# Performance work log

Hardware: AMD Instinct MI355X
Metric: run time of the kernel (lower is better)

## Reference

```python
import jax, jax.numpy as jnp
import numpy as np

NUM_ROUTES = 3
EPS = 1e-8

def _squash(s):
    # s: [b, out_caps, out_dim]
    n = jnp.linalg.norm(s, axis=-1, keepdims=True)
    scale = n ** 2 / (1.0 + n ** 2)
    return scale * (s / (n + EPS))

def setup_inputs() -> dict:
    key = jax.random.key(0)
    kx, kw = jax.random.split(key)
    B, IN_CAPS, IN_DIM, OUT_CAPS, OUT_DIM = 32, 2048, 16, 64, 32
    x = jax.random.normal(kx, (B, IN_CAPS, IN_DIM), dtype=jnp.float32)
    W = jax.random.normal(kw, (1, IN_CAPS, OUT_CAPS, OUT_DIM, IN_DIM), dtype=jnp.float32)
    return {"x": x, "W": W}

def reference(x, W):
    # u_hat[b,i,o,d] = sum_k W[0,i,o,d,k] * x[b,i,k]
    u_hat = jnp.einsum('iodk,bik->biod', W[0], x)  # [B, in_caps, out_caps, out_dim]
    b_ij = jnp.zeros(u_hat.shape[:3], dtype=u_hat.dtype)  # [B, in_caps, out_caps]
    v_j = None
    for _ in range(NUM_ROUTES):
        c_ij = jax.nn.softmax(b_ij, axis=2)
        s_j = jnp.einsum('bio,biod->bod', c_ij, u_hat)  # weighted sum over in_caps
        v_j = _squash(s_j)
        agreement = jnp.einsum('biod,bod->bio', u_hat, v_j)
        b_ij = b_ij + agreement
    return v_j
```

## Files before the change

### kernel.cpp

```cpp
#include <hip/hip_runtime.h>
#include <cstdint>

#define NB 32
#define IC 2048
#define IK 16
#define OC 64
#define OD 32
#define ODF (OC*OD)
#define PARTBLK (16*ODF)
#define NCH 128
#define NSLOT (NCH*2)

typedef __fp16 h2 __attribute__((ext_vector_type(2)));
typedef __fp16 h8 __attribute__((ext_vector_type(8)));
typedef float  f4 __attribute__((ext_vector_type(4)));

__device__ __forceinline__ h2 pk2(float a, float b) {
#if __has_builtin(__builtin_amdgcn_cvt_pkrtz)
  return __builtin_amdgcn_cvt_pkrtz(a, b);
#else
  h2 r; r.x = (__fp16)a; r.y = (__fp16)b; return r;
#endif
}
__device__ __forceinline__ float fdot2a(h2 a, h2 b, float c) {
#if __has_builtin(__builtin_amdgcn_fdot2)
  return __builtin_amdgcn_fdot2(a, b, c, false);
#else
  return c + (float)a.x*(float)b.x + (float)a.y*(float)b.y;
#endif
}
__device__ __forceinline__ unsigned int bcu(h2 v){ return __builtin_bit_cast(unsigned int, v); }
__device__ __forceinline__ h2 bch2(unsigned int u){ return __builtin_bit_cast(h2, u); }
__device__ __forceinline__ h8 bch8(uint4 u){ return __builtin_bit_cast(h8, u); }
__device__ __forceinline__ f4 mfma_16x16x32(h8 a, h8 b, f4 c) {
  return __builtin_amdgcn_mfma_f32_16x16x32_f16(a, b, c, 0, 0, 0);
}
__device__ __forceinline__ uint4 packw(const float* wp) {
  const float4 wa = *(const float4*)wp;
  const float4 wb = *(const float4*)(wp + 4);
  uint4 au;
  au.x = bcu(pk2(wa.x, wa.y)); au.y = bcu(pk2(wa.z, wa.w));
  au.z = bcu(pk2(wb.x, wb.y)); au.w = bcu(pk2(wb.z, wb.w));
  return au;
}


template<int WH>
__global__ __launch_bounds__(1024)
void caps_gemm0(const float* __restrict__ xg, const float* __restrict__ Wg,
                uint4* __restrict__ Whg, float* __restrict__ part)
{
  __shared__ uint4 x_h[8][2][16];
  const int t = threadIdx.x, w = t >> 6, l = t & 63, lb = l & 15, lg = l >> 4;
  const int bid = blockIdx.x, slot = bid >> 3;
  const int bh = slot & 1;
  const int ci = (bid & 7)*16 + (slot >> 1);
  const int i0 = ci*16, bg0 = bh*16;
  const f4 zf = {0.f,0.f,0.f,0.f};
  f4 acc[8];
#pragma unroll
  for (int q = 0; q < 8; ++q) acc[q] = zf;

  for (int g8 = 0; g8 < 16; g8 += 8) {
    if (g8) __syncthreads();
    if (t < 256) {
      const int si = t >> 5, kc2 = (t >> 4) & 1, sb = t & 15;
      const float* xp = &xg[((size_t)(bg0 + sb)*IC + (i0 + g8 + si))*IK + kc2*8];
      x_h[si][kc2][sb] = packw(xp);
    }
    __syncthreads();
#pragma unroll 1
    for (int p = 0; p < 4; ++p) {
      const int isel = lg >> 1, kc = lg & 1, il = p*2 + isel;
      const h8 B = bch8(x_h[il][kc][lb]);
#pragma unroll
      for (int tt = 0; tt < 8; ++tt) {
        const size_t widx = (size_t)(i0 + g8 + il)*ODF + (w*8 + tt)*16 + lb;
        const uint4 au = packw(&Wg[widx*IK + kc*8]);
        if (WH && bh == 0) Whg[widx*2 + kc] = au;
        acc[tt] = mfma_16x16x32(bch8(au), B, acc[tt]);
      }
    }
  }
  float* pp = part + (size_t)(ci*2 + bh)*PARTBLK;
#pragma unroll
  for (int tt = 0; tt < 8; ++tt) {
    float4 st;
    st.x = acc[tt].x*(1.f/64.f); st.y = acc[tt].y*(1.f/64.f);
    st.z = acc[tt].z*(1.f/64.f); st.w = acc[tt].w*(1.f/64.f);
    *(float4*)&pp[(size_t)lb*ODF + (w*8 + tt)*16 + lg*4] = st;
  }
}

template<int ITER, int WH>
__global__ __launch_bounds__(1024)
void caps_agree(const float* __restrict__ xg, const float* __restrict__ Wg,
                const uint4* __restrict__ Whg, const float* __restrict__ vin,
                float* __restrict__ a1g, float* __restrict__ cg)
{
  __shared__ uint4 x_h[8][2][16];
  __shared__ float agr[8*64*17];
  const int t = threadIdx.x, w = t >> 6, l = t & 63, lb = l & 15, lg = l >> 4;
  const int bid = blockIdx.x, slot = bid >> 3;
  const int bh = slot & 1;
  const int ci8 = (bid & 7)*32 + (slot >> 1);
  const int i0 = ci8*8, bg0 = bh*16;
  const f4 zf = {0.f,0.f,0.f,0.f};

  if (t < 256) {
    const int si = t >> 5, kc2 = (t >> 4) & 1, sb = t & 15;
    const float* xp = &xg[((size_t)(bg0 + sb)*IC + (i0 + si))*IK + kc2*8];
    x_h[si][kc2][sb] = packw(xp);
  }
  unsigned int vh[16];
#pragma unroll
  for (int tt = 0; tt < 8; ++tt) {
    const int o = w*4 + (tt >> 1);
    const float4 vv = *(const float4*)
      &vin[((size_t)(bg0 + lb)*OC + o)*OD + (tt & 1)*16 + lg*4];
    vh[tt*2]   = bcu(pk2(0.5f*vv.x, 0.5f*vv.y));
    vh[tt*2+1] = bcu(pk2(0.5f*vv.z, 0.5f*vv.w));
  }
  __syncthreads();

  const int isel = lg >> 1, kc = lg & 1;
  const unsigned int msk = (lg >= 2) ? 0x80008000u : 0u;

#pragma unroll 1
  for (int p = 0; p < 4; ++p) {
    const int iA = i0 + p*2, iB = iA + 1;
    const uint4 bu = x_h[p*2 + isel][kc][lb];
    uint4 bm;
    bm.x = bu.x^msk; bm.y = bu.y^msk; bm.z = bu.z^msk; bm.w = bu.w^msk;
    const h8 Bp = bch8(bu), Bm = bch8(bm);
    float ap1[4] = {0.f,0.f,0.f,0.f}, ap2[4] = {0.f,0.f,0.f,0.f};
#pragma unroll
    for (int tt = 0; tt < 8; ++tt) {
      const size_t widx = (size_t)(iA + isel)*ODF + (w*8 + tt)*16 + lb;
      const uint4 au = WH ? Whg[widx*2 + kc] : packw(&Wg[widx*IK + kc*8]);
      const h8 A = bch8(au);
      const f4 s = mfma_16x16x32(A, Bp, zf);
      const f4 d = mfma_16x16x32(A, Bm, zf);
      const h2 sh0 = pk2(s.x, s.y), sh1 = pk2(s.z, s.w);
      const h2 dh0 = pk2(d.x, d.y), dh1 = pk2(d.z, d.w);
      const float ds = fdot2a(sh0, bch2(vh[tt*2]), fdot2a(sh1, bch2(vh[tt*2+1]), 0.f));
      const float dd = fdot2a(dh0, bch2(vh[tt*2]), fdot2a(dh1, bch2(vh[tt*2+1]), 0.f));
      ap1[tt >> 1] += ds + dd;
      ap2[tt >> 1] += ds - dd;
    }
#pragma unroll
    for (int q = 0; q < 4; ++q) {
      float a1v = ap1[q], a2v = ap2[q];
      a1v += __shfl_xor(a1v, 16); a1v += __shfl_xor(a1v, 32);
      a2v += __shfl_xor(a2v, 16); a2v += __shfl_xor(a2v, 32);
      if (l < 16) {
        const int o = w*4 + q;
        float b1 = a1v, b2 = a2v;
        if (ITER == 2) {
          b1 += a1g[((size_t)iA*OC + o)*NB + bg0 + lb];
          b2 += a1g[((size_t)iB*OC + o)*NB + bg0 + lb];
        }
        if (ITER == 1) {
          a1g[((size_t)iA*OC + o)*NB + bg0 + lb] = b1;
          a1g[((size_t)iB*OC + o)*NB + bg0 + lb] = b2;
        }
        agr[((p*2)*64 + o)*17 + lb]   = b1;
        agr[((p*2+1)*64 + o)*17 + lb] = b2;
      }
    }
  }
  __syncthreads();
#pragma unroll
  for (int r = 0; r < 8; ++r) {
    const int row = w*8 + r, si = row >> 4, b = row & 15;
    const float a = agr[(si*64 + l)*17 + b];
    float m = a;
#pragma unroll
    for (int off = 1; off < 64; off <<= 1) m = fmaxf(m, __shfl_xor(m, off));
    const float e = __expf(a - m);
    float se = e;
#pragma unroll
    for (int off = 1; off < 64; off <<= 1) se += __shfl_xor(se, off);
    agr[(si*64 + l)*17 + b] = e / se;
  }
  __syncthreads();
#pragma unroll
  for (int cc = 0; cc < 8; ++cc) {
    const int o = t >> 4, b2 = t & 15;
    cg[((size_t)(i0 + cc)*OC + o)*NB + bg0 + b2] = agr[(cc*64 + o)*17 + b2];
  }
}

template<int WH>
__global__ __launch_bounds__(1024)
void caps_saccum(const float* __restrict__ xg, const float* __restrict__ Wg,
                 const uint4* __restrict__ Whg, const float* __restrict__ cg,
                 float* __restrict__ part)
{
  __shared__ uint4 x_h[8][2][16];
  const int t = threadIdx.x, w = t >> 6, l = t & 63, lb = l & 15, lg = l >> 4;
  const int bid = blockIdx.x, slot = bid >> 3;
  const int bh = slot & 1;
  const int ci = (bid & 7)*16 + (slot >> 1);
  const int i0 = ci*16, bg0 = bh*16;
  const f4 zf = {0.f,0.f,0.f,0.f};
  f4 acc[8];
#pragma unroll
  for (int q = 0; q < 8; ++q) acc[q] = zf;
  const int isel = lg >> 1, kc = lg & 1;

  for (int g8 = 0; g8 < 16; g8 += 8) {
    if (g8) __syncthreads();
    if (t < 256) {
      const int si = t >> 5, kc2 = (t >> 4) & 1, sb = t & 15;
      const float* xp = &xg[((size_t)(bg0 + sb)*IC + (i0 + g8 + si))*IK + kc2*8];
      x_h[si][kc2][sb] = packw(xp);
    }
    __syncthreads();
#pragma unroll 1
    for (int p = 0; p < 4; ++p) {
      const int iA = i0 + g8 + p*2, iB = iA + 1;
      const uint4 bu = x_h[p*2 + isel][kc][lb];
#pragma unroll
      for (int q = 0; q < 4; ++q) {
        const int o = w*4 + q;
        const float c1 = cg[((size_t)iA*OC + o)*NB + bg0 + lb];
        const float c2 = cg[((size_t)iB*OC + o)*NB + bg0 + lb];
        const float cs = (lg < 2) ? c1 : c2;
        const h2 cpk = pk2(cs, cs);
        uint4 bs;
        bs.x = bcu(bch2(bu.x)*cpk); bs.y = bcu(bch2(bu.y)*cpk);
        bs.z = bcu(bch2(bu.z)*cpk); bs.w = bcu(bch2(bu.w)*cpk);
        const h8 Bs = bch8(bs);
#pragma unroll
        for (int th = 0; th < 2; ++th) {
          const int tt = q*2 + th;
          const size_t widx = (size_t)(iA + isel)*ODF + (w*8 + tt)*16 + lb;
          const uint4 au = WH ? Whg[widx*2 + kc] : packw(&Wg[widx*IK + kc*8]);
          acc[tt] = mfma_16x16x32(bch8(au), Bs, acc[tt]);
        }
      }
    }
  }
  float* pp = part + (size_t)(ci*2 + bh)*PARTBLK;
#pragma unroll
  for (int tt = 0; tt < 8; ++tt) {
    float4 st; st.x = acc[tt].x; st.y = acc[tt].y; st.z = acc[tt].z; st.w = acc[tt].w;
    *(float4*)&pp[(size_t)lb*ODF + (w*8 + tt)*16 + lg*4] = st;
  }
}

__global__ __launch_bounds__(64)
void caps_reduce(const float* __restrict__ part, float* __restrict__ vout)
{
  const int r  = blockIdx.x;
  const int b  = r >> 6, o = r & 63;
  const int bh = b >> 4, bl = b & 15;
  const int d  = threadIdx.x & 31;
  const int h  = threadIdx.x >> 5;
  const float* p = part + (size_t)bh*PARTBLK + (size_t)bl*ODF + o*OD + d;
  float s = 0.f;
#pragma unroll 4
  for (int q = 0; q < NCH/2; ++q)
    s += p[(size_t)((h*(NCH/2) + q)*2)*PARTBLK];
  s += __shfl_xor(s, 32);
  float n2 = s*s;
#pragma unroll
  for (int off = 1; off < 32; off <<= 1) n2 += __shfl_xor(n2, off);
  const float n = sqrtf(n2);
  const float f = n2 / ((1.f + n2)*(n + 1e-8f));
  if (h == 0) vout[(size_t)r*OD + d] = s*f;
}

extern "C" void kernel_launch(void* const* d_in, const int* in_sizes, int n_in,
                              void* d_out, int out_size, void* d_ws, size_t ws_size,
                              hipStream_t stream)
{
  const float* xg = (const float*)d_in[0];
  const float* Wg = (const float*)d_in[1];
  float* out = (float*)d_out;

  const size_t part_b = (size_t)NSLOT*PARTBLK*sizeof(float);
  const size_t a1_b   = (size_t)IC*OC*NB*sizeof(float);
  const size_t c_b    = a1_b;
  const size_t v_b    = (size_t)NB*ODF*sizeof(float);
  const size_t wh_b   = (size_t)IC*ODF*IK*2;

  char* ws = (char*)d_ws;
  float* part = (float*)ws;                  ws += part_b;
  float* a1g  = (float*)ws;                  ws += a1_b;
  float* cg   = (float*)ws;                  ws += c_b;
  float* vbuf = (float*)ws;                  ws += v_b;
  uint4* whg  = (uint4*)ws;
  const bool WH = (part_b + a1_b + c_b + v_b + wh_b) <= ws_size;

  if (WH) {
    caps_gemm0<1><<<NSLOT, 1024, 0, stream>>>(xg, Wg, whg, part);
    caps_reduce<<<NB*OC, 64, 0, stream>>>(part, vbuf);
    caps_agree<1,1><<<512, 1024, 0, stream>>>(xg, Wg, whg, vbuf, a1g, cg);
    caps_saccum<1><<<NSLOT, 1024, 0, stream>>>(xg, Wg, whg, cg, part);
    caps_reduce<<<NB*OC, 64, 0, stream>>>(part, vbuf);
    caps_agree<2,1><<<512, 1024, 0, stream>>>(xg, Wg, whg, vbuf, a1g, cg);
    caps_saccum<1><<<NSLOT, 1024, 0, stream>>>(xg, Wg, whg, cg, part);
    caps_reduce<<<NB*OC, 64, 0, stream>>>(part, out);
  } else {
    caps_gemm0<0><<<NSLOT, 1024, 0, stream>>>(xg, Wg, nullptr, part);
    caps_reduce<<<NB*OC, 64, 0, stream>>>(part, vbuf);
    caps_agree<1,0><<<512, 1024, 0, stream>>>(xg, Wg, nullptr, vbuf, a1g, cg);
    caps_saccum<0><<<NSLOT, 1024, 0, stream>>>(xg, Wg, nullptr, cg, part);
    caps_reduce<<<NB*OC, 64, 0, stream>>>(part, vbuf);
    caps_agree<2,0><<<512, 1024, 0, stream>>>(xg, Wg, nullptr, vbuf, a1g, cg);
    caps_saccum<0><<<NSLOT, 1024, 0, stream>>>(xg, Wg, nullptr, cg, part);
    caps_reduce<<<NB*OC, 64, 0, stream>>>(part, out);
  }
}
```

Baseline: 286.7 us.

## Retile caps_saccum so each block covers all 32 batches over a quarter of outputs

caps_saccum changes from blocks covering 16 batches by all 64 output capsules to blocks covering all 32 batches by a quarter of the output tiles, with 512 blocks instead of 256. Each W fragment loaded from memory now feeds two MFMAs, one per batch half, so global W traffic per useful FLOP is halved. The partial-sum layout becomes 128 chunks of 32 batches, and caps_reduce gains a second mode to read it. The cost is that each block computes fewer MFMA tiles per wave and per-element c scaling is repeated per batch half.

New measurement: 290.9 us. No clear change (+1.5%).

```diff
diff --git a/kernel.cpp b/kernel.cpp
--- a/kernel.cpp
+++ b/kernel.cpp
@@ -7,9 +7,11 @@
 #define OC 64
 #define OD 32
 #define ODF (OC*OD)
-#define PARTBLK (16*ODF)
-#define NCH 128
-#define NSLOT (NCH*2)
+#define PARTBLK16 (16*ODF)
+#define PARTBLK32 (32*ODF)
+#define NCH0 128
+#define NCHA 256
+#define NCHS 128
 
 typedef __fp16 h2 __attribute__((ext_vector_type(2)));
 typedef __fp16 h8 __attribute__((ext_vector_type(8)));
@@ -82,7 +84,7 @@
       }
     }
   }
-  float* pp = part + (size_t)(ci*2 + bh)*PARTBLK;
+  float* pp = part + (size_t)(ci*2 + bh)*PARTBLK16;
 #pragma unroll
   for (int tt = 0; tt < 8; ++tt) {
     float4 st;
@@ -197,72 +199,84 @@
                  const uint4* __restrict__ Whg, const float* __restrict__ cg,
                  float* __restrict__ part)
 {
-  __shared__ uint4 x_h[8][2][16];
+  __shared__ uint4 x_h[8][2][32];
   const int t = threadIdx.x, w = t >> 6, l = t & 63, lb = l & 15, lg = l >> 4;
-  const int bid = blockIdx.x, slot = bid >> 3;
-  const int bh = slot & 1;
-  const int ci = (bid & 7)*16 + (slot >> 1);
-  const int i0 = ci*16, bg0 = bh*16;
+  const int ci = blockIdx.x >> 2;
+  const int oq = blockIdx.x & 3;
+  const int i0 = ci*16;
   const f4 zf = {0.f,0.f,0.f,0.f};
-  f4 acc[8];
-#pragma unroll
-  for (int q = 0; q < 8; ++q) acc[q] = zf;
+  f4 acc[2][2];
+  acc[0][0] = zf; acc[0][1] = zf; acc[1][0] = zf; acc[1][1] = zf;
   const int isel = lg >> 1, kc = lg & 1;
+  const int tile0 = oq*32 + w*2;
 
   for (int g8 = 0; g8 < 16; g8 += 8) {
     if (g8) __syncthreads();
-    if (t < 256) {
-      const int si = t >> 5, kc2 = (t >> 4) & 1, sb = t & 15;
-      const float* xp = &xg[((size_t)(bg0 + sb)*IC + (i0 + g8 + si))*IK + kc2*8];
-      x_h[si][kc2][sb] = packw(xp);
+    if (t < 512) {
+      const int si = t >> 6, kc2 = (t >> 5) & 1, sb = t & 31;
+      x_h[si][kc2][sb] = packw(&xg[((size_t)sb*IC + (i0 + g8 + si))*IK + kc2*8]);
     }
     __syncthreads();
 #pragma unroll 1
     for (int p = 0; p < 4; ++p) {
       const int iA = i0 + g8 + p*2, iB = iA + 1;
-      const uint4 bu = x_h[p*2 + isel][kc][lb];
-#pragma unroll
-      for (int q = 0; q < 4; ++q) {
-        const int o = w*4 + q;
-        const float c1 = cg[((size_t)iA*OC + o)*NB + bg0 + lb];
-        const float c2 = cg[((size_t)iB*OC + o)*NB + bg0 + lb];
-        const float cs = (lg < 2) ? c1 : c2;
-        const h2 cpk = pk2(cs, cs);
-        uint4 bs;
-        bs.x = bcu(bch2(bu.x)*cpk); bs.y = bcu(bch2(bu.y)*cpk);
-        bs.z = bcu(bch2(bu.z)*cpk); bs.w = bcu(bch2(bu.w)*cpk);
-        const h8 Bs = bch8(bs);
-#pragma unroll
-        for (int th = 0; th < 2; ++th) {
-          const int tt = q*2 + th;
-          const size_t widx = (size_t)(iA + isel)*ODF + (w*8 + tt)*16 + lb;
-          const uint4 au = WH ? Whg[widx*2 + kc] : packw(&Wg[widx*IK + kc*8]);
-          acc[tt] = mfma_16x16x32(bch8(au), Bs, acc[tt]);
+      uint4 bu[2];
+      bu[0] = x_h[p*2 + isel][kc][lb];
+      bu[1] = x_h[p*2 + isel][kc][16 + lb];
+#pragma unroll
+      for (int tt = 0; tt < 2; ++tt) {
+        const int tile = tile0 + tt;
+        const int o = tile >> 1;
+        const size_t widx = (size_t)(iA + isel)*ODF + tile*16 + lb;
+        const uint4 au = WH ? Whg[widx*2 + kc] : packw(&Wg[widx*IK + kc*8]);
+        const h8 A = bch8(au);
+#pragma unroll
+        for (int b2 = 0; b2 < 2; ++b2) {
+          const int b = b2*16 + lb;
+          const float c1 = cg[((size_t)iA*OC + o)*NB + b];
+          const float c2 = cg[((size_t)iB*OC + o)*NB + b];
+          const float cs = (lg < 2) ? c1 : c2;
+          const h2 cpk = pk2(cs, cs);
+          uint4 bs;
+          bs.x = bcu(bch2(bu[b2].x)*cpk); bs.y = bcu(bch2(bu[b2].y)*cpk);
+          bs.z = bcu(bch2(bu[b2].z)*cpk); bs.w = bcu(bch2(bu[b2].w)*cpk);
+          acc[tt][b2] = mfma_16x16x32(A, bch8(bs), acc[tt][b2]);
         }
       }
     }
   }
-  float* pp = part + (size_t)(ci*2 + bh)*PARTBLK;
-#pragma unroll
-  for (int tt = 0; tt < 8; ++tt) {
-    float4 st; st.x = acc[tt].x; st.y = acc[tt].y; st.z = acc[tt].z; st.w = acc[tt].w;
-    *(float4*)&pp[(size_t)lb*ODF + (w*8 + tt)*16 + lg*4] = st;
-  }
-}
-
+  float* pp = part + (size_t)ci*PARTBLK32;
+#pragma unroll
+  for (int tt = 0; tt < 2; ++tt)
+#pragma unroll
+    for (int b2 = 0; b2 < 2; ++b2) {
+      const f4 a = acc[tt][b2];
+      float4 st; st.x = a.x; st.y = a.y; st.z = a.z; st.w = a.w;
+      *(float4*)&pp[(size_t)(b2*16 + lb)*ODF + (tile0 + tt)*16 + lg*4] = st;
+    }
+}
+
+template<int MODE>
 __global__ __launch_bounds__(64)
 void caps_reduce(const float* __restrict__ part, float* __restrict__ vout)
 {
   const int r  = blockIdx.x;
   const int b  = r >> 6, o = r & 63;
-  const int bh = b >> 4, bl = b & 15;
   const int d  = threadIdx.x & 31;
   const int h  = threadIdx.x >> 5;
-  const float* p = part + (size_t)bh*PARTBLK + (size_t)bl*ODF + o*OD + d;
   float s = 0.f;
+  if (MODE == 0) {
+    const int bh = b >> 4, bl = b & 15;
+    const float* p = part + (size_t)bh*PARTBLK16 + (size_t)bl*ODF + o*OD + d;
 #pragma unroll 4
-  for (int q = 0; q < NCH/2; ++q)
-    s += p[(size_t)((h*(NCH/2) + q)*2)*PARTBLK];
+    for (int q = 0; q < 64; ++q)
+      s += p[(size_t)((h*64 + q)*2)*PARTBLK16];
+  } else {
+    const float* p = part + (size_t)b*ODF + o*OD + d;
+#pragma unroll 4
+    for (int q = 0; q < 64; ++q)
+      s += p[(size_t)(h*64 + q)*PARTBLK32];
+  }
   s += __shfl_xor(s, 32);
   float n2 = s*s;
 #pragma unroll
@@ -280,7 +294,7 @@
   const float* Wg = (const float*)d_in[1];
   float* out = (float*)d_out;
 
-  const size_t part_b = (size_t)NSLOT*PARTBLK*sizeof(float);
+  const size_t part_b = (size_t)NCHS*PARTBLK32*sizeof(float);
   const size_t a1_b   = (size_t)IC*OC*NB*sizeof(float);
   const size_t c_b    = a1_b;
   const size_t v_b    = (size_t)NB*ODF*sizeof(float);
@@ -295,22 +309,22 @@
   const bool WH = (part_b + a1_b + c_b + v_b + wh_b) <= ws_size;
 
   if (WH) {
-    caps_gemm0<1><<<NSLOT, 1024, 0, stream>>>(xg, Wg, whg, part);
-    caps_reduce<<<NB*OC, 64, 0, stream>>>(part, vbuf);
-    caps_agree<1,1><<<512, 1024, 0, stream>>>(xg, Wg, whg, vbuf, a1g, cg);
-    caps_saccum<1><<<NSLOT, 1024, 0, stream>>>(xg, Wg, whg, cg, part);
-    caps_reduce<<<NB*OC, 64, 0, stream>>>(part, vbuf);
-    caps_agree<2,1><<<512, 1024, 0, stream>>>(xg, Wg, whg, vbuf, a1g, cg);
-    caps_saccum<1><<<NSLOT, 1024, 0, stream>>>(xg, Wg, whg, cg, part);
-    caps_reduce<<<NB*OC, 64, 0, stream>>>(part, out);
+    caps_gemm0<1><<<NCH0*2, 1024, 0, stream>>>(xg, Wg, whg, part);
+    caps_reduce<0><<<NB*OC, 64, 0, stream>>>(part, vbuf);
+    caps_agree<1,1><<<NCHA*2, 1024, 0, stream>>>(xg, Wg, whg, vbuf, a1g, cg);
+    caps_saccum<1><<<NCHS*4, 1024, 0, stream>>>(xg, Wg, whg, cg, part);
+    caps_reduce<1><<<NB*OC, 64, 0, stream>>>(part, vbuf);
+    caps_agree<2,1><<<NCHA*2, 1024, 0, stream>>>(xg, Wg, whg, vbuf, a1g, cg);
+    caps_saccum<1><<<NCHS*4, 1024, 0, stream>>>(xg, Wg, whg, cg, part);
+    caps_reduce<1><<<NB*OC, 64, 0, stream>>>(part, out);
   } else {
-    caps_gemm0<0><<<NSLOT, 1024, 0, stream>>>(xg, Wg, nullptr, part);
-    caps_reduce<<<NB*OC, 64, 0, stream>>>(part, vbuf);
-    caps_agree<1,0><<<512, 1024, 0, stream>>>(xg, Wg, nullptr, vbuf, a1g, cg);
-    caps_saccum<0><<<NSLOT, 1024, 0, stream>>>(xg, Wg, nullptr, cg, part);
-    caps_reduce<<<NB*OC, 64, 0, stream>>>(part, vbuf);
-    caps_agree<2,0><<<512, 1024, 0, stream>>>(xg, Wg, nullptr, vbuf, a1g, cg);
-    caps_saccum<0><<<NSLOT, 1024, 0, stream>>>(xg, Wg, nullptr, cg, part);
-    caps_reduce<<<NB*OC, 64, 0, stream>>>(part, out);
-  }
-}
+    caps_gemm0<0><<<NCH0*2, 1024, 0, stream>>>(xg, Wg, nullptr, part);
+    caps_reduce<0><<<NB*OC, 64, 0, stream>>>(part, vbuf);
+    caps_agree<1,0><<<NCHA*2, 1024, 0, stream>>>(xg, Wg, nullptr, vbuf, a1g, cg);
+    caps_saccum<0><<<NCHS*4, 1024, 0, stream>>>(xg, Wg, nullptr, cg, part);
+    caps_reduce<1><<<NB*OC, 64, 0, stream>>>(part, vbuf);
+    caps_agree<2,0><<<NCHA*2, 1024, 0, stream>>>(xg, Wg, nullptr, vbuf, a1g, cg);
+    caps_saccum<0><<<NCHS*4, 1024, 0, stream>>>(xg, Wg, nullptr, cg, part);
+    caps_reduce<1><<<NB*OC, 64, 0, stream>>>(part, out);
+  }
+}
```
